# Performance work log

Hardware: AMD Instinct MI355X
Metric: run time of the kernel (lower is better)

Reference implementation:

```python
import jax, jax.numpy as jnp
import numpy as np

N, V, F, H, B, HID = 256, 32, 128, 8, 8, 64
R_MAX = 5.0
DH = F // H


def fc_edges(n):
    a = np.arange(n)
    s, r = np.meshgrid(a, a, indexing="ij")
    m = s != r
    return jnp.asarray(s[m]), jnp.asarray(r[m])

SENDERS, RECEIVERS = fc_edges(N)
E = N * (N - 1)


def sph_harmonics(u):
    # u: [..., 3] unit vectors -> [..., 15] = l=1(3)+l=2(5)+l=3(7), e3nn 'component' normalization
    x, y, z = u[..., 0], u[..., 1], u[..., 2]
    s3 = 3.0 ** 0.5; s5 = 5.0 ** 0.5; s7 = 7.0 ** 0.5
    s15 = 15.0 ** 0.5; s105 = 105.0 ** 0.5
    s35_8 = (35.0 / 8.0) ** 0.5; s21_8 = (21.0 / 8.0) ** 0.5
    l1 = [s3 * y, s3 * z, s3 * x]
    l2 = [s15 * x * y, s15 * y * z, 0.5 * s5 * (3 * z * z - 1),
          s15 * x * z, 0.5 * s15 * (x * x - y * y)]
    l3 = [s35_8 * y * (3 * x * x - y * y), s105 * x * y * z,
          s21_8 * y * (5 * z * z - 1), 0.5 * s7 * z * (5 * z * z - 3),
          s21_8 * x * (5 * z * z - 1), 0.5 * s105 * z * (x * x - y * y),
          s35_8 * x * (x * x - 3 * y * y)]
    return jnp.stack(l1 + l2 + l3, axis=-1)


def radial_embed(lengths):
    # Bessel basis (e3nn.bessel) times soft envelope (e3nn.soft_envelope)
    x = jnp.maximum(lengths, 1e-6)[..., None]
    k = jnp.arange(1, B + 1, dtype=lengths.dtype)
    bes = (2.0 / R_MAX) ** 0.5 * jnp.sin(k * jnp.pi * x / R_MAX) / x
    def sus(t):
        return jnp.where(t > 0, jnp.exp(-1.0 / jnp.where(t > 0, t, 1.0)), 0.0)
    env = 1.2 * sus(2.0 * (1.0 - lengths / R_MAX)) / sus(jnp.asarray(2.0))
    return bes * env[..., None]


def setup_inputs():
    key = jax.random.key(0)
    ks = jax.random.split(key, 16)
    def w(k, shape):
        return jax.random.normal(k, shape, jnp.float32) / (shape[0] ** 0.5)
    D_edge = 2 * F + V * B
    return {
        "positions": jax.random.normal(ks[0], (N, V, 3), jnp.float32),
        "features": jax.random.normal(ks[1], (N, F), jnp.float32),
        "We1": w(ks[2], (D_edge, HID)), "be1": jnp.zeros((HID,), jnp.float32),
        "We2": w(ks[3], (HID, HID)), "be2": jnp.zeros((HID,), jnp.float32),
        "W_q": w(ks[4], (F, F)), "W_k": w(ks[5], (HID, F)),
        "W_v": w(ks[6], (F, F)), "W_vec": w(ks[7], (HID, V)),
        "W_mix": w(ks[8], (V, V)),
        "M1": w(ks[9], (F, HID)), "bm1": jnp.zeros((HID,), jnp.float32),
        "M2": w(ks[10], (HID, HID)), "bm2": jnp.zeros((HID,), jnp.float32),
        "M3": w(ks[11], (HID, F)), "bm3": jnp.zeros((F,), jnp.float32),
    }


def reference(positions, features, We1, be1, We2, be2, W_q, W_k, W_v, W_vec,
              W_mix, M1, bm1, M2, bm2, M3, bm3):
    act = jax.nn.selu
    s, r = SENDERS, RECEIVERS
    vectors = positions[s] - positions[r]                        # [E, V, 3]
    lengths = jnp.sqrt(jnp.sum(vectors * vectors, -1) + 1e-18)   # [E, V] safe_norm
    unit = vectors / lengths[..., None]
    sph = sph_harmonics(unit)                                    # [E, V, 15]
    radial = radial_embed(lengths).reshape(E, V * B)             # [E, V*B]
    edge_weight_cutoff = jnp.ones((E,), positions.dtype)

    # edge MLP on invariants (radial embedding + src/dst scalar features)
    edge_in = jnp.concatenate([features[s], features[r], radial], -1)
    h = act(edge_in @ We1 + be1)
    h = act(h @ We2 + be2)                                       # [E, HID]

    # multi-head attention over incoming edges per node (segment softmax)
    q = (features @ W_q).reshape(N, H, DH)
    k = (h @ W_k).reshape(E, H, DH)
    logit = jnp.einsum("ehd,ehd->eh", k, q[r]) / (DH ** 0.5)
    lmax = jax.ops.segment_max(logit, r, num_segments=N)
    ex = edge_weight_cutoff[:, None] * jnp.exp(logit - lmax[r])
    denom = jax.ops.segment_sum(ex, r, num_segments=N)
    alpha = ex / (denom[r] + 1e-12)                              # [E, H]

    # invariant (0e) values
    v = (features[s] @ W_v).reshape(E, H, DH)
    inv_agg = jax.ops.segment_sum(alpha[..., None] * v, r, num_segments=N).reshape(N, F)

    # equivariant (1o) values: scalar-gated l=1 spherical harmonics (sqrt(3)*unit)
    coeff = h @ W_vec                                            # [E, V]
    alpha_v = jnp.repeat(alpha, V // H, axis=1)                  # [E, V]
    vec_msg = ((alpha_v * coeff) * (3.0 ** 0.5))[..., None] * unit  # [E, V, 3]
    vec_agg = jax.ops.segment_sum(vec_msg, r, num_segments=N)    # [N, V, 3]
    vec_out = jnp.einsum("nvc,vw->nwc", vec_agg, W_mix)

    # final invariant MLP + residuals
    hi = act(inv_agg @ M1 + bm1)
    hi = act(hi @ M2 + bm2)
    inv_out = hi @ M3 + bm3
    return (vec_out + positions, inv_out + features)
```

## Files before the change

kernel.cpp:

```cpp
#include <hip/hip_runtime.h>
#include <hip/hip_bf16.h>

#define NN 256
#define VC 32
#define FD 128

typedef unsigned int uint32;
typedef unsigned short u16;
typedef __attribute__((ext_vector_type(8))) short bf16x8;
typedef __attribute__((ext_vector_type(4))) float f32x4;

__device__ __forceinline__ float selu_f(float x) {
    const float lam = 1.0507009873554805f;
    const float la  = 1.7580993408473766f;
    return x > 0.f ? lam * x : la * (__expf(x) - 1.f);
}

__device__ __forceinline__ u16 f32_to_bf16_rne(float f) {
    uint32 u = __float_as_uint(f);
    uint32 r = (u + 0x7fffu + ((u >> 16) & 1u)) >> 16;
    return (u16)r;
}

__device__ __forceinline__ float bf16_to_f32(u16 h) {
    return __uint_as_float(((uint32)h) << 16);
}

struct Params {
    const float *pos, *feat, *We1, *be1, *We2, *be2, *Wq, *Wk, *Wv, *Wvec,
                *Wmix, *M1, *bm1, *M2, *bm2, *M3, *bm3;
    float *A, *Bf;
    u16 *kqb, *w1b, *we2b, *wvb, *fvtH, *fvtL, *ptH, *ptL;
    float *lgg2;
    u16 *cfg2;
    float *stats;
    float *inv, *vec4;
    float *out0, *out1;
};

__global__ __launch_bounds__(256) void k1_pre(Params P)
{
    __shared__ float fl[FD];
    __shared__ float ql[FD];
    const int vb = blockIdx.x;
    const int t = threadIdx.x;
    if (vb < 256) {
        const int n = vb;
        {
            const int gid = n*256 + t;
            if (gid < 16384) {
                const int c = gid >> 8, k = gid & 255;
                P.w1b[gid] = f32_to_bf16_rne(P.We1[(256 + k)*64 + c]);
            } else if (gid < 20480) {
                const int o = gid - 16384;
                const int c = o >> 6, k = o & 63;
                P.we2b[o] = f32_to_bf16_rne(P.We2[k*64 + c]);
            } else if (gid < 22528) {
                const int o = gid - 20480;
                const int v = o >> 6, k = o & 63;
                P.wvb[o] = f32_to_bf16_rne(P.Wvec[k*32 + v]);
            }
        }
        if (t < FD) fl[t] = P.feat[n*FD + t];
        __syncthreads();
        if (t < 64) {
            float a = 0.f;
            for (int i = 0; i < FD; ++i) a = fmaf(fl[i], P.We1[i*64 + t], a);
            P.A[n*64 + t] = a;
        } else if (t < 128) {
            const int j = t - 64;
            float a = P.be1[j];
            for (int i = 0; i < FD; ++i) a = fmaf(fl[i], P.We1[(FD+i)*64 + j], a);
            P.Bf[n*64 + j] = a;
        } else {
            const int j = t - 128;
            float a = 0.f;
            for (int i = 0; i < FD; ++i) a = fmaf(fl[i], P.Wq[i*FD + j], a);
            ql[j] = a * 0.25f;
        }
        if (t < 8)  P.lgg2[n*2048 + t*256 + n] = -1e30f;
        if (t < 32) P.cfg2[(size_t)n*8192 + t*256 + n] = 0;
        __syncthreads();
        for (int o = t; o < 512; o += 256) {
            const int h = o >> 6, j = o & 63;
            float a = 0.f;
            #pragma unroll
            for (int d = 0; d < 16; ++d)
                a = fmaf(P.Wk[j*FD + h*16 + d], ql[h*16 + d], a);
            P.kqb[n*512 + o] = f32_to_bf16_rne(a);
        }
    } else {
        const int n = vb - 256;
        if (t < FD) fl[t] = P.feat[n*FD + t];
        __syncthreads();
        if (t < FD) {
            float a = 0.f;
            for (int i = 0; i < FD; ++i) a = fmaf(fl[i], P.Wv[i*FD + t], a);
            const u16 hi = f32_to_bf16_rne(a);
            const u16 lo = f32_to_bf16_rne(a - bf16_to_f32(hi));
            P.fvtH[t*256 + n] = hi;
            P.fvtL[t*256 + n] = lo;
            const int v = t >> 2, c = t & 3;
            const float val = (c < 3) ? P.pos[(n*VC + v)*3 + c] : 1.0f;
            const u16 phi = f32_to_bf16_rne(val);
            const u16 plo = f32_to_bf16_rne(val - bf16_to_f32(phi));
            P.ptH[(v*4+c)*256 + n] = phi;
            P.ptL[(v*4+c)*256 + n] = plo;
        }
    }
}

__global__ __launch_bounds__(256) void k2_edge(Params P)
{
    __shared__ u16 rad[8192];
    __shared__ u16 h1b[2048];
    __shared__ u16 h2b[2048];
    __shared__ float invl[1056];
    __shared__ float pm[2][8];
    __shared__ float psv[2][8];

    const int t = threadIdx.x;
    const int wave = t >> 6, l = t & 63;
    const int li = l & 15, q = l >> 4;
    const int mh = wave >> 1, eh = wave & 1;
    const int r = blockIdx.x >> 1, tpart = blockIdx.x & 1;
    const int e = eh*16 + li;
    const int swz16 = (e & 7) << 3;

    bf16x8 w1A[2][8];
    #pragma unroll
    for (int mt = 0; mt < 2; ++mt) {
        const int c = mh*32 + mt*16 + li;
        #pragma unroll
        for (int kb = 0; kb < 8; ++kb)
            w1A[mt][kb] = *(const bf16x8*)(P.w1b + c*256 + kb*32 + q*8);
    }
    bf16x8 we2A[2][2];
    #pragma unroll
    for (int mt = 0; mt < 2; ++mt) {
        const int c2 = mh*32 + mt*16 + li;
        #pragma unroll
        for (int kb = 0; kb < 2; ++kb)
            we2A[mt][kb] = *(const bf16x8*)(P.we2b + c2*64 + kb*32 + q*8);
    }
    bf16x8 wvA[2];
    {
        const int v = mh*16 + li;
        #pragma unroll
        for (int kb = 0; kb < 2; ++kb)
            wvA[kb] = *(const bf16x8*)(P.wvb + v*64 + kb*32 + q*8);
    }
    bf16x8 kqA[2];
    if (li < 8) {
        #pragma unroll
        for (int kb = 0; kb < 2; ++kb)
            kqA[kb] = *(const bf16x8*)(P.kqb + r*512 + li*64 + kb*32 + q*8);
    } else {
        #pragma unroll
        for (int kb = 0; kb < 2; ++kb)
            #pragma unroll
            for (int j = 0; j < 8; ++j) kqA[kb][j] = 0;
    }
    float bfreg[2][4], be2reg[2][4];
    #pragma unroll
    for (int mt = 0; mt < 2; ++mt)
        #pragma unroll
        for (int rg = 0; rg < 4; ++rg) {
            const int c = mh*32 + mt*16 + q*4 + rg;
            bfreg[mt][rg] = P.Bf[r*64 + c];
            be2reg[mt][rg] = P.be2[c];
        }

    float m_run[4], s_run[4];
    #pragma unroll
    for (int rg = 0; rg < 4; ++rg) { m_run[rg] = -3.0e38f; s_run[rg] = 0.f; }

    for (int it = 0; it < 4; ++it) {
        const int s0 = (tpart*4 + it) * 32;
        const int sp = s0 + e;
        int s = sp + (sp >= r ? 1 : 0); if (s > 255) s = 255;
        __syncthreads();

        float As[2][4];
        #pragma unroll
        for (int mt = 0; mt < 2; ++mt)
            #pragma unroll
            for (int rg = 0; rg < 4; ++rg)
                As[mt][rg] = P.A[s*64 + mh*32 + mt*16 + q*4 + rg];

        {
            const int ep = t & 31, vg = t >> 5;
            const int spp = s0 + ep;
            int sv = spp + (spp >= r ? 1 : 0); if (sv > 255) sv = 255;
            #pragma unroll
            for (int kk = 0; kk < 4; ++kk) {
                const int v = vg*4 + kk;
                const float* ps = P.pos + (sv*VC + v)*3;
                const float* pr = P.pos + (r*VC + v)*3;
                const float dx = ps[0]-pr[0], dy = ps[1]-pr[1], dz = ps[2]-pr[2];
                const float d2 = fmaf(dx,dx,fmaf(dy,dy,dz*dz)) + 1e-18f;
                const float len = sqrtf(d2);
                invl[ep*33 + v] = rsqrtf(d2);
                const float x = fmaxf(len, 1e-6f);
                const float tt2 = 2.f - 0.4f*len;
                const float env = tt2 > 0.f ? 1.9784655248401538f * __expf(-1.f/tt2) : 0.f;
                const float coefc = 0.6324555320336759f * env / x;
                float s_cur, c1;
                __sincosf(0.6283185307179586f * x, &s_cur, &c1);
                const float c2x = 2.f * c1;
                float s_prev = 0.f;
                union { uint4 u4; u16 us[8]; } pk;
                #pragma unroll
                for (int bb = 0; bb < 8; ++bb) {
                    pk.us[bb] = f32_to_bf16_rne(coefc * s_cur);
                    const float s_next = fmaf(c2x, s_cur, -s_prev);
                    s_prev = s_cur; s_cur = s_next;
                }
                *(uint4*)((char*)rad + ((ep*512 + v*16) ^ ((ep & 15) << 4))) = pk.u4;
            }
        }
        __syncthreads();

        f32x4 d1[2] = {{0.f,0.f,0.f,0.f},{0.f,0.f,0.f,0.f}};
        #pragma unroll
        for (int kb = 0; kb < 8; ++kb) {
            const bf16x8 rf = *(const bf16x8*)((const char*)rad +
                                ((e*512 + (kb*4+q)*16) ^ ((e & 15) << 4)));
            d1[0] = __builtin_amdgcn_mfma_f32_16x16x32_bf16(w1A[0][kb], rf, d1[0], 0, 0, 0);
            d1[1] = __builtin_amdgcn_mfma_f32_16x16x32_bf16(w1A[1][kb], rf, d1[1], 0, 0, 0);
        }
        #pragma unroll
        for (int mt = 0; mt < 2; ++mt) {
            const int c0 = mh*32 + mt*16 + q*4;
            const u16 p0 = f32_to_bf16_rne(selu_f(d1[mt][0] + As[mt][0] + bfreg[mt][0]));
            const u16 p1 = f32_to_bf16_rne(selu_f(d1[mt][1] + As[mt][1] + bfreg[mt][1]));
            const u16 p2 = f32_to_bf16_rne(selu_f(d1[mt][2] + As[mt][2] + bfreg[mt][2]));
            const u16 p3 = f32_to_bf16_rne(selu_f(d1[mt][3] + As[mt][3] + bfreg[mt][3]));
            *(uint32*)&h1b[e*64 + ((c0)     ^ swz16)] = (uint32)p0 | ((uint32)p1 << 16);
            *(uint32*)&h1b[e*64 + ((c0 + 2) ^ swz16)] = (uint32)p2 | ((uint32)p3 << 16);
        }
        __syncthreads();

        f32x4 d2[2] = {{0.f,0.f,0.f,0.f},{0.f,0.f,0.f,0.f}};
        #pragma unroll
        for (int kb = 0; kb < 2; ++kb) {
            const bf16x8 hb = *(const bf16x8*)&h1b[e*64 + ((kb*32 + q*8) ^ swz16)];
            d2[0] = __builtin_amdgcn_mfma_f32_16x16x32_bf16(we2A[0][kb], hb, d2[0], 0, 0, 0);
            d2[1] = __builtin_amdgcn_mfma_f32_16x16x32_bf16(we2A[1][kb], hb, d2[1], 0, 0, 0);
        }
        #pragma unroll
        for (int mt = 0; mt < 2; ++mt) {
            const int c0 = mh*32 + mt*16 + q*4;
            const u16 p0 = f32_to_bf16_rne(selu_f(d2[mt][0] + be2reg[mt][0]));
            const u16 p1 = f32_to_bf16_rne(selu_f(d2[mt][1] + be2reg[mt][1]));
            const u16 p2 = f32_to_bf16_rne(selu_f(d2[mt][2] + be2reg[mt][2]));
            const u16 p3 = f32_to_bf16_rne(selu_f(d2[mt][3] + be2reg[mt][3]));
            *(uint32*)&h2b[e*64 + ((c0)     ^ swz16)] = (uint32)p0 | ((uint32)p1 << 16);
            *(uint32*)&h2b[e*64 + ((c0 + 2) ^ swz16)] = (uint32)p2 | ((uint32)p3 << 16);
        }
        __syncthreads();

        f32x4 d3 = {0.f,0.f,0.f,0.f};
        f32x4 dl = {0.f,0.f,0.f,0.f};
        #pragma unroll
        for (int kb = 0; kb < 2; ++kb) {
            const bf16x8 hb = *(const bf16x8*)&h2b[e*64 + ((kb*32 + q*8) ^ swz16)];
            d3 = __builtin_amdgcn_mfma_f32_16x16x32_bf16(wvA[kb], hb, d3, 0, 0, 0);
            if (mh == 0)
                dl = __builtin_amdgcn_mfma_f32_16x16x32_bf16(kqA[kb], hb, dl, 0, 0, 0);
        }
        if (sp < 255) {
            #pragma unroll
            for (int rg = 0; rg < 4; ++rg) {
                const int v = mh*16 + q*4 + rg;
                P.cfg2[(size_t)r*8192 + v*256 + s] =
                    f32_to_bf16_rne(d3[rg] * 1.7320508075688772f * invl[e*33 + v]);
            }
            if (mh == 0 && q < 2) {
                #pragma unroll
                for (int rg = 0; rg < 4; ++rg) {
                    const float lgv = dl[rg];
                    P.lgg2[(size_t)r*2048 + (q*4+rg)*256 + s] = lgv;
                    const float mo = m_run[rg];
                    if (lgv > mo) {
                        s_run[rg] = fmaf(s_run[rg], __expf(mo - lgv), 1.f);
                        m_run[rg] = lgv;
                    } else {
                        s_run[rg] += __expf(lgv - mo);
                    }
                }
            }
        }
    }

    if (mh == 0 && q < 2) {
        #pragma unroll
        for (int rg = 0; rg < 4; ++rg) {
            float m = m_run[rg], sv = s_run[rg];
            #pragma unroll
            for (int mask = 1; mask <= 8; mask <<= 1) {
                const float mo = __shfl_xor(m, mask);
                const float so = __shfl_xor(sv, mask);
                const float mn = fmaxf(m, mo);
                sv = sv*__expf(m - mn) + so*__expf(mo - mn);
                m = mn;
            }
            if (li == 0) { pm[eh][q*4+rg] = m; psv[eh][q*4+rg] = sv; }
        }
    }
    __syncthreads();
    if (t < 8) {
        const float m0 = pm[0][t], m1 = pm[1][t];
        const float s0v = psv[0][t], s1v = psv[1][t];
        const float m = fmaxf(m0, m1);
        const float sv = s0v*__expf(m0 - m) + s1v*__expf(m1 - m);
        P.stats[((r*2 + tpart)*8 + t)*2 + 0] = m;
        P.stats[((r*2 + tpart)*8 + t)*2 + 1] = sv;
    }
}

__global__ __launch_bounds__(64) void k3b_agg(Params P)
{
    const int l = threadIdx.x, li = l & 15, q = l >> 4;
    const int task = blockIdx.x;
    int r0, hh, v = 0;
    const bool isInv = (task < 128);
    if (isInv) { hh = task >> 4; r0 = (task & 15) * 16; }
    else { const int b2 = task - 128; v = b2 >> 4; r0 = (b2 & 15) * 16; hh = v >> 2; }

    const float2 st0 = *(const float2*)&P.stats[(((r0+li)*2 + 0)*8 + hh)*2];
    const float2 st1 = *(const float2*)&P.stats[(((r0+li)*2 + 1)*8 + hh)*2];
    const float mx = fmaxf(st0.x, st1.x);
    const float den = st0.y*__expf(st0.x - mx) + st1.y*__expf(st1.x - mx);
    const float invden = 1.f / (den + 1e-12f);

    if (isInv) {
        bf16x8 fH[8], fL[8];
        #pragma unroll
        for (int kb = 0; kb < 8; ++kb) {
            fH[kb] = *(const bf16x8*)(P.fvtH + (hh*16+li)*256 + kb*32 + q*8);
            fL[kb] = *(const bf16x8*)(P.fvtL + (hh*16+li)*256 + kb*32 + q*8);
        }
        const float* lgr = P.lgg2 + (size_t)(r0+li)*2048 + hh*256;
        f32x4 Ch = {0.f,0.f,0.f,0.f};
        f32x4 Cl = {0.f,0.f,0.f,0.f};
        #pragma unroll
        for (int kb = 0; kb < 8; ++kb) {
            const float4 g0 = *(const float4*)(lgr + kb*32 + q*8);
            const float4 g1 = *(const float4*)(lgr + kb*32 + q*8 + 4);
            bf16x8 a;
            a[0] = (short)f32_to_bf16_rne(__expf(g0.x-mx));
            a[1] = (short)f32_to_bf16_rne(__expf(g0.y-mx));
            a[2] = (short)f32_to_bf16_rne(__expf(g0.z-mx));
            a[3] = (short)f32_to_bf16_rne(__expf(g0.w-mx));
            a[4] = (short)f32_to_bf16_rne(__expf(g1.x-mx));
            a[5] = (short)f32_to_bf16_rne(__expf(g1.y-mx));
            a[6] = (short)f32_to_bf16_rne(__expf(g1.z-mx));
            a[7] = (short)f32_to_bf16_rne(__expf(g1.w-mx));
            Ch = __builtin_amdgcn_mfma_f32_16x16x32_bf16(a, fH[kb], Ch, 0, 0, 0);
            Cl = __builtin_amdgcn_mfma_f32_16x16x32_bf16(a, fL[kb], Cl, 0, 0, 0);
        }
        #pragma unroll
        for (int rg = 0; rg < 4; ++rg) {
            const float d = __shfl(invden, q*4 + rg);
            P.inv[(r0 + q*4 + rg)*128 + hh*16 + li] = (Ch[rg] + Cl[rg]) * d;
        }
    } else {
        bf16x8 pH[8], pL[8];
        #pragma unroll
        for (int kb = 0; kb < 8; ++kb) {
            if (li < 4) {
                pH[kb] = *(const bf16x8*)(P.ptH + (v*4+li)*256 + kb*32 + q*8);
                pL[kb] = *(const bf16x8*)(P.ptL + (v*4+li)*256 + kb*32 + q*8);
            } else {
                #pragma unroll
                for (int j = 0; j < 8; ++j) { pH[kb][j] = 0; pL[kb][j] = 0; }
            }
        }
        const float* lgr = P.lgg2 + (size_t)(r0+li)*2048 + hh*256;
        const u16*  cfr = P.cfg2 + (size_t)(r0+li)*8192 + v*256;
        f32x4 Ch = {0.f,0.f,0.f,0.f};
        f32x4 Cl = {0.f,0.f,0.f,0.f};
        #pragma unroll
        for (int kb = 0; kb < 8; ++kb) {
            const float4 g0 = *(const float4*)(lgr + kb*32 + q*8);
            const float4 g1 = *(const float4*)(lgr + kb*32 + q*8 + 4);
            const bf16x8 cf8 = *(const bf16x8*)(cfr + kb*32 + q*8);
            bf16x8 a;
            a[0] = (short)f32_to_bf16_rne(__expf(g0.x-mx) * bf16_to_f32((u16)cf8[0]));
            a[1] = (short)f32_to_bf16_rne(__expf(g0.y-mx) * bf16_to_f32((u16)cf8[1]));
            a[2] = (short)f32_to_bf16_rne(__expf(g0.z-mx) * bf16_to_f32((u16)cf8[2]));
            a[3] = (short)f32_to_bf16_rne(__expf(g0.w-mx) * bf16_to_f32((u16)cf8[3]));
            a[4] = (short)f32_to_bf16_rne(__expf(g1.x-mx) * bf16_to_f32((u16)cf8[4]));
            a[5] = (short)f32_to_bf16_rne(__expf(g1.y-mx) * bf16_to_f32((u16)cf8[5]));
            a[6] = (short)f32_to_bf16_rne(__expf(g1.z-mx) * bf16_to_f32((u16)cf8[6]));
            a[7] = (short)f32_to_bf16_rne(__expf(g1.w-mx) * bf16_to_f32((u16)cf8[7]));
            Ch = __builtin_amdgcn_mfma_f32_16x16x32_bf16(a, pH[kb], Ch, 0, 0, 0);
            Cl = __builtin_amdgcn_mfma_f32_16x16x32_bf16(a, pL[kb], Cl, 0, 0, 0);
        }
        #pragma unroll
        for (int rg = 0; rg < 4; ++rg) {
            const float d = __shfl(invden, q*4 + rg);
            if (li < 4)
                P.vec4[(r0 + q*4 + rg)*128 + v*4 + li] = (Ch[rg] + Cl[rg]) * d;
        }
    }
}

__global__ __launch_bounds__(256) void k3c_out(Params P)
{
    __shared__ float part[4][64];
    __shared__ float inva[128];
    __shared__ float vec4s[128];
    __shared__ float pos96[96];
    __shared__ float vecl[96];
    __shared__ float hi1[64];
    __shared__ float hi2[64];
    const int r = blockIdx.x;
    const int t = threadIdx.x;
    if (t < 128) inva[t] = P.inv[r*128 + t];
    else         vec4s[t-128] = P.vec4[r*128 + (t-128)];
    if (t < 96)  pos96[t] = P.pos[r*96 + t];
    __syncthreads();
    if (t < 96) {
        const int v = t / 3, c = t - v*3;
        vecl[t] = vec4s[v*4 + c] - vec4s[v*4 + 3] * pos96[t];
    }
    {
        const int f = t & 63, g = t >> 6;
        const int k0 = g*32;
        float acc = 0.f;
        #pragma unroll 8
        for (int k = k0; k < k0 + 32; ++k)
            acc = fmaf(inva[k], P.M1[k*64 + f], acc);
        part[g][f] = acc;
    }
    __syncthreads();
    if (t < 64) {
        const float a1 = P.bm1[t] + part[0][t] + part[1][t] + part[2][t] + part[3][t];
        hi1[t] = selu_f(a1);
    }
    __syncthreads();
    if (t < 64) {
        float a2 = P.bm2[t];
        #pragma unroll 8
        for (int k = 0; k < 64; ++k) a2 = fmaf(hi1[k], P.M2[k*64 + t], a2);
        hi2[t] = selu_f(a2);
    }
    __syncthreads();
    if (t < 128) {
        float a = P.bm3[t];
        #pragma unroll 8
        for (int k = 0; k < 64; ++k) a = fmaf(hi2[k], P.M3[k*128 + t], a);
        P.out1[r*128 + t] = a + P.feat[r*128 + t];
    } else if (t < 224) {
        const int o = t - 128;
        const int w = o / 3, c = o - w*3;
        float a = 0.f;
        #pragma unroll
        for (int v = 0; v < 32; ++v)
            a = fmaf(vecl[v*3 + c], P.Wmix[v*32 + w], a);
        P.out0[r*96 + o] = a + pos96[o];
    }
}

extern "C" void kernel_launch(void* const* d_in, const int* in_sizes, int n_in,
                              void* d_out, int out_size, void* d_ws, size_t ws_size,
                              hipStream_t stream)
{
    char* ws = (char*)d_ws;
    if (ws_size < (size_t)7024640) return;

    Params p;
    p.pos  = (const float*)d_in[0];
    p.feat = (const float*)d_in[1];
    p.We1  = (const float*)d_in[2];
    p.be1  = (const float*)d_in[3];
    p.We2  = (const float*)d_in[4];
    p.be2  = (const float*)d_in[5];
    p.Wq   = (const float*)d_in[6];
    p.Wk   = (const float*)d_in[7];
    p.Wv   = (const float*)d_in[8];
    p.Wvec = (const float*)d_in[9];
    p.Wmix = (const float*)d_in[10];
    p.M1   = (const float*)d_in[11];
    p.bm1  = (const float*)d_in[12];
    p.M2   = (const float*)d_in[13];
    p.bm2  = (const float*)d_in[14];
    p.M3   = (const float*)d_in[15];
    p.bm3  = (const float*)d_in[16];

    p.A    = (float*)(ws + 0);
    p.Bf   = (float*)(ws + 65536);
    p.kqb  = (u16*)(ws + 131072);
    p.w1b  = (u16*)(ws + 393216);
    p.we2b = (u16*)(ws + 425984);
    p.wvb  = (u16*)(ws + 434176);
    p.fvtH = (u16*)(ws + 438272);
    p.fvtL = (u16*)(ws + 503808);
    p.ptH  = (u16*)(ws + 569344);
    p.ptL  = (u16*)(ws + 634880);
    p.lgg2 = (float*)(ws + 700416);
    p.cfg2 = (u16*)(ws + 2797568);
    p.stats = (float*)(ws + 6991872);
    p.inv  = (float*)(ws + 0);
    p.vec4 = (float*)(ws + 131072);

    p.out0 = (float*)d_out;
    p.out1 = p.out0 + NN*VC*3;

    hipLaunchKernelGGL(k1_pre,  dim3(512), dim3(256), 0, stream, p);
    hipLaunchKernelGGL(k2_edge, dim3(512), dim3(256), 0, stream, p);
    hipLaunchKernelGGL(k3b_agg, dim3(640), dim3(64),  0, stream, p);
    hipLaunchKernelGGL(k3c_out, dim3(256), dim3(256), 0, stream, p);
}
```

Baseline: 45.58 us.

## Fuse aggregation and output MLP into one per-receiver fp32 kernel

Merges the MFMA-based aggregation kernel into the output kernel. Each block now builds attention weights for one receiver in shared memory, and the invariant and vector aggregation is done with fp32 FMA dot products over fp32 value and position tables. This drops the bf16 hi/lo split encoding and removes one launch plus the intermediate inv/vec4 round trip through global memory. In exchange it gives up matrix-core use and cuts the aggregation grid from 640 small blocks to 256, and every block rereads the full 128x256 fvt and pt tables from global memory.

```diff
diff --git a/kernel.cpp b/kernel.cpp
--- a/kernel.cpp
+++ b/kernel.cpp
@@ -30,11 +30,11 @@
     const float *pos, *feat, *We1, *be1, *We2, *be2, *Wq, *Wk, *Wv, *Wvec,
                 *Wmix, *M1, *bm1, *M2, *bm2, *M3, *bm3;
     float *A, *Bf;
-    u16 *kqb, *w1b, *we2b, *wvb, *fvtH, *fvtL, *ptH, *ptL;
+    u16 *kqb, *w1b, *we2b, *wvb;
+    float *fvt, *pt;
     float *lgg2;
     u16 *cfg2;
     float *stats;
-    float *inv, *vec4;
     float *out0, *out1;
 };
 
@@ -96,16 +96,9 @@
         if (t < FD) {
             float a = 0.f;
             for (int i = 0; i < FD; ++i) a = fmaf(fl[i], P.Wv[i*FD + t], a);
-            const u16 hi = f32_to_bf16_rne(a);
-            const u16 lo = f32_to_bf16_rne(a - bf16_to_f32(hi));
-            P.fvtH[t*256 + n] = hi;
-            P.fvtL[t*256 + n] = lo;
+            P.fvt[t*256 + n] = a;
             const int v = t >> 2, c = t & 3;
-            const float val = (c < 3) ? P.pos[(n*VC + v)*3 + c] : 1.0f;
-            const u16 phi = f32_to_bf16_rne(val);
-            const u16 plo = f32_to_bf16_rne(val - bf16_to_f32(phi));
-            P.ptH[(v*4+c)*256 + n] = phi;
-            P.ptL[(v*4+c)*256 + n] = plo;
+            P.pt[t*256 + n] = (c < 3) ? P.pos[(n*VC + v)*3 + c] : 1.0f;
         }
     }
 }
@@ -319,108 +312,82 @@
     }
 }
 
-__global__ __launch_bounds__(64) void k3b_agg(Params P)
+__global__ __launch_bounds__(256) void k3_fused(Params P)
 {
-    const int l = threadIdx.x, li = l & 15, q = l >> 4;
-    const int task = blockIdx.x;
-    int r0, hh, v = 0;
-    const bool isInv = (task < 128);
-    if (isInv) { hh = task >> 4; r0 = (task & 15) * 16; }
-    else { const int b2 = task - 128; v = b2 >> 4; r0 = (b2 & 15) * 16; hh = v >> 2; }
-
-    const float2 st0 = *(const float2*)&P.stats[(((r0+li)*2 + 0)*8 + hh)*2];
-    const float2 st1 = *(const float2*)&P.stats[(((r0+li)*2 + 1)*8 + hh)*2];
-    const float mx = fmaxf(st0.x, st1.x);
-    const float den = st0.y*__expf(st0.x - mx) + st1.y*__expf(st1.x - mx);
-    const float invden = 1.f / (den + 1e-12f);
-
-    if (isInv) {
-        bf16x8 fH[8], fL[8];
-        #pragma unroll
-        for (int kb = 0; kb < 8; ++kb) {
-            fH[kb] = *(const bf16x8*)(P.fvtH + (hh*16+li)*256 + kb*32 + q*8);
-            fL[kb] = *(const bf16x8*)(P.fvtL + (hh*16+li)*256 + kb*32 + q*8);
-        }
-        const float* lgr = P.lgg2 + (size_t)(r0+li)*2048 + hh*256;
-        f32x4 Ch = {0.f,0.f,0.f,0.f};
-        f32x4 Cl = {0.f,0.f,0.f,0.f};
-        #pragma unroll
-        for (int kb = 0; kb < 8; ++kb) {
-            const float4 g0 = *(const float4*)(lgr + kb*32 + q*8);
-            const float4 g1 = *(const float4*)(lgr + kb*32 + q*8 + 4);
-            bf16x8 a;
-            a[0] = (short)f32_to_bf16_rne(__expf(g0.x-mx));
-            a[1] = (short)f32_to_bf16_rne(__expf(g0.y-mx));
-            a[2] = (short)f32_to_bf16_rne(__expf(g0.z-mx));
-            a[3] = (short)f32_to_bf16_rne(__expf(g0.w-mx));
-            a[4] = (short)f32_to_bf16_rne(__expf(g1.x-mx));
-            a[5] = (short)f32_to_bf16_rne(__expf(g1.y-mx));
-            a[6] = (short)f32_to_bf16_rne(__expf(g1.z-mx));
-            a[7] = (short)f32_to_bf16_rne(__expf(g1.w-mx));
-            Ch = __builtin_amdgcn_mfma_f32_16x16x32_bf16(a, fH[kb], Ch, 0, 0, 0);
-            Cl = __builtin_amdgcn_mfma_f32_16x16x32_bf16(a, fL[kb], Cl, 0, 0, 0);
-        }
-        #pragma unroll
-        for (int rg = 0; rg < 4; ++rg) {
-            const float d = __shfl(invden, q*4 + rg);
-            P.inv[(r0 + q*4 + rg)*128 + hh*16 + li] = (Ch[rg] + Cl[rg]) * d;
-        }
-    } else {
-        bf16x8 pH[8], pL[8];
-        #pragma unroll
-        for (int kb = 0; kb < 8; ++kb) {
-            if (li < 4) {
-                pH[kb] = *(const bf16x8*)(P.ptH + (v*4+li)*256 + kb*32 + q*8);
-                pL[kb] = *(const bf16x8*)(P.ptL + (v*4+li)*256 + kb*32 + q*8);
-            } else {
-                #pragma unroll
-                for (int j = 0; j < 8; ++j) { pH[kb][j] = 0; pL[kb][j] = 0; }
-            }
-        }
-        const float* lgr = P.lgg2 + (size_t)(r0+li)*2048 + hh*256;
-        const u16*  cfr = P.cfg2 + (size_t)(r0+li)*8192 + v*256;
-        f32x4 Ch = {0.f,0.f,0.f,0.f};
-        f32x4 Cl = {0.f,0.f,0.f,0.f};
-        #pragma unroll
-        for (int kb = 0; kb < 8; ++kb) {
-            const float4 g0 = *(const float4*)(lgr + kb*32 + q*8);
-            const float4 g1 = *(const float4*)(lgr + kb*32 + q*8 + 4);
-            const bf16x8 cf8 = *(const bf16x8*)(cfr + kb*32 + q*8);
-            bf16x8 a;
-            a[0] = (short)f32_to_bf16_rne(__expf(g0.x-mx) * bf16_to_f32((u16)cf8[0]));
-            a[1] = (short)f32_to_bf16_rne(__expf(g0.y-mx) * bf16_to_f32((u16)cf8[1]));
-            a[2] = (short)f32_to_bf16_rne(__expf(g0.z-mx) * bf16_to_f32((u16)cf8[2]));
-            a[3] = (short)f32_to_bf16_rne(__expf(g0.w-mx) * bf16_to_f32((u16)cf8[3]));
-            a[4] = (short)f32_to_bf16_rne(__expf(g1.x-mx) * bf16_to_f32((u16)cf8[4]));
-            a[5] = (short)f32_to_bf16_rne(__expf(g1.y-mx) * bf16_to_f32((u16)cf8[5]));
-            a[6] = (short)f32_to_bf16_rne(__expf(g1.z-mx) * bf16_to_f32((u16)cf8[6]));
-            a[7] = (short)f32_to_bf16_rne(__expf(g1.w-mx) * bf16_to_f32((u16)cf8[7]));
-            Ch = __builtin_amdgcn_mfma_f32_16x16x32_bf16(a, pH[kb], Ch, 0, 0, 0);
-            Cl = __builtin_amdgcn_mfma_f32_16x16x32_bf16(a, pL[kb], Cl, 0, 0, 0);
-        }
-        #pragma unroll
-        for (int rg = 0; rg < 4; ++rg) {
-            const float d = __shfl(invden, q*4 + rg);
-            if (li < 4)
-                P.vec4[(r0 + q*4 + rg)*128 + v*4 + li] = (Ch[rg] + Cl[rg]) * d;
-        }
-    }
-}
-
-__global__ __launch_bounds__(256) void k3c_out(Params P)
-{
-    __shared__ float part[4][64];
+    __shared__ float alT[8][260];
+    __shared__ float wmT[32][260];
+    __shared__ float smx[8], sinvd[8];
+    __shared__ float invp[256];
+    __shared__ float vecp[256];
     __shared__ float inva[128];
     __shared__ float vec4s[128];
     __shared__ float pos96[96];
     __shared__ float vecl[96];
     __shared__ float hi1[64];
     __shared__ float hi2[64];
+    __shared__ float part[4][64];
     const int r = blockIdx.x;
     const int t = threadIdx.x;
-    if (t < 128) inva[t] = P.inv[r*128 + t];
-    else         vec4s[t-128] = P.vec4[r*128 + (t-128)];
-    if (t < 96)  pos96[t] = P.pos[r*96 + t];
+
+    if (t < 8) {
+        const float2 s0 = *(const float2*)&P.stats[((r*2 + 0)*8 + t)*2];
+        const float2 s1 = *(const float2*)&P.stats[((r*2 + 1)*8 + t)*2];
+        const float m = fmaxf(s0.x, s1.x);
+        const float den = s0.y*__expf(s0.x - m) + s1.y*__expf(s1.x - m);
+        smx[t] = m;
+        sinvd[t] = 1.f / (den + 1e-12f);
+    }
+    if (t < 96) pos96[t] = P.pos[r*96 + t];
+    __syncthreads();
+    {
+        const float* lgr = P.lgg2 + (size_t)r*2048;
+        const u16*  cfr = P.cfg2 + (size_t)r*8192;
+        float al8[8];
+        #pragma unroll
+        for (int h = 0; h < 8; ++h) {
+            al8[h] = __expf(lgr[h*256 + t] - smx[h]) * sinvd[h];
+            alT[h][t] = al8[h];
+        }
+        #pragma unroll
+        for (int v = 0; v < 32; ++v)
+            wmT[v][t] = al8[v>>2] * bf16_to_f32(cfr[v*256 + t]);
+    }
+    __syncthreads();
+    {
+        const int f = t & 127, half = t >> 7, h = f >> 4;
+        const float4* fr4 = (const float4*)(P.fvt + f*256 + half*128);
+        const float4* ar4 = (const float4*)(&alT[h][half*128]);
+        float a0 = 0.f, a1 = 0.f;
+        #pragma unroll 8
+        for (int s4 = 0; s4 < 32; s4 += 2) {
+            const float4 f0 = fr4[s4],   av0 = ar4[s4];
+            const float4 f1 = fr4[s4+1], av1 = ar4[s4+1];
+            a0 = fmaf(av0.x, f0.x, a0); a0 = fmaf(av0.y, f0.y, a0);
+            a0 = fmaf(av0.z, f0.z, a0); a0 = fmaf(av0.w, f0.w, a0);
+            a1 = fmaf(av1.x, f1.x, a1); a1 = fmaf(av1.y, f1.y, a1);
+            a1 = fmaf(av1.z, f1.z, a1); a1 = fmaf(av1.w, f1.w, a1);
+        }
+        invp[t] = a0 + a1;
+    }
+    {
+        const int o = t & 127, half = t >> 7, v = o >> 2;
+        const float4* pr4 = (const float4*)(P.pt + o*256 + half*128);
+        const float4* wr4 = (const float4*)(&wmT[v][half*128]);
+        float a0 = 0.f, a1 = 0.f;
+        #pragma unroll 8
+        for (int s4 = 0; s4 < 32; s4 += 2) {
+            const float4 p0 = pr4[s4],   wv0 = wr4[s4];
+            const float4 p1 = pr4[s4+1], wv1 = wr4[s4+1];
+            a0 = fmaf(wv0.x, p0.x, a0); a0 = fmaf(wv0.y, p0.y, a0);
+            a0 = fmaf(wv0.z, p0.z, a0); a0 = fmaf(wv0.w, p0.w, a0);
+            a1 = fmaf(wv1.x, p1.x, a1); a1 = fmaf(wv1.y, p1.y, a1);
+            a1 = fmaf(wv1.z, p1.z, a1); a1 = fmaf(wv1.w, p1.w, a1);
+        }
+        vecp[t] = a0 + a1;
+    }
+    __syncthreads();
+    if (t < 128) inva[t] = invp[t] + invp[128 + t];
+    else { const int o = t - 128; vec4s[o] = vecp[o] + vecp[128 + o]; }
     __syncthreads();
     if (t < 96) {
         const int v = t / 3, c = t - v*3;
@@ -496,21 +463,16 @@
     p.w1b  = (u16*)(ws + 393216);
     p.we2b = (u16*)(ws + 425984);
     p.wvb  = (u16*)(ws + 434176);
-    p.fvtH = (u16*)(ws + 438272);
-    p.fvtL = (u16*)(ws + 503808);
-    p.ptH  = (u16*)(ws + 569344);
-    p.ptL  = (u16*)(ws + 634880);
+    p.fvt  = (float*)(ws + 438272);
+    p.pt   = (float*)(ws + 569344);
     p.lgg2 = (float*)(ws + 700416);
     p.cfg2 = (u16*)(ws + 2797568);
     p.stats = (float*)(ws + 6991872);
-    p.inv  = (float*)(ws + 0);
-    p.vec4 = (float*)(ws + 131072);
 
     p.out0 = (float*)d_out;
     p.out1 = p.out0 + NN*VC*3;
 
-    hipLaunchKernelGGL(k1_pre,  dim3(512), dim3(256), 0, stream, p);
-    hipLaunchKernelGGL(k2_edge, dim3(512), dim3(256), 0, stream, p);
-    hipLaunchKernelGGL(k3b_agg, dim3(640), dim3(64),  0, stream, p);
-    hipLaunchKernelGGL(k3c_out, dim3(256), dim3(256), 0, stream, p);
-}
+    hipLaunchKernelGGL(k1_pre,   dim3(512), dim3(256), 0, stream, p);
+    hipLaunchKernelGGL(k2_edge,  dim3(512), dim3(256), 0, stream, p);
+    hipLaunchKernelGGL(k3_fused, dim3(256), dim3(256), 0, stream, p);
+}
```

After: 48.87 us. 7.2% more time.
